# Optimization experiments

Hardware: AMD Instinct MI355X
Metric: run time of the kernel (lower is better)

## Reference

```python
import jax, jax.numpy as jnp
import numpy as np
import math

N_HEAD = 16
ROPE_BASE = 10000.0


def _rope_cos_sin(seq_len, head_dim, dtype):
    # standard RoPE tables: freqs_i = base^(-2i/d), i in [0, d/2)
    half = head_dim // 2
    inv_freq = ROPE_BASE ** (-(jnp.arange(half, dtype=jnp.float32) * 2.0 / head_dim))
    t = jnp.arange(seq_len, dtype=jnp.float32)
    ang = t[:, None] * inv_freq[None, :]  # [S, d/2]
    return jnp.cos(ang).astype(dtype), jnp.sin(ang).astype(dtype)


def _apply_rope(x, cos, sin):
    # x: [B, S, H, d]; rotate interleaved even/odd pairs
    x1 = x[..., 0::2]
    x2 = x[..., 1::2]
    c = cos[None, :, None, :]
    s = sin[None, :, None, :]
    out = jnp.stack([x1 * c - x2 * s, x1 * s + x2 * c], axis=-1)
    return out.reshape(x.shape)


def setup_inputs() -> dict:
    key = jax.random.key(0)
    kx, kq, kk, kv, ko = jax.random.split(key, 5)
    B, S, H = 2, 2048, 1024
    x = jax.random.normal(kx, (B, S, H), dtype=jnp.float32)
    scale = 0.02
    w_q = jax.random.normal(kq, (H, H), dtype=jnp.float32) * scale
    w_k = jax.random.normal(kk, (H, H), dtype=jnp.float32) * scale
    w_v = jax.random.normal(kv, (H, H), dtype=jnp.float32) * scale
    w_o = jax.random.normal(ko, (H, H), dtype=jnp.float32) * scale
    return {"x": x, "w_q": w_q, "w_k": w_k, "w_v": w_v, "w_o": w_o}


def reference(x, w_q, w_k, w_v, w_o):
    B, S, H = x.shape
    d = H // N_HEAD
    # torch nn.Linear(bias=False): y = x @ W^T, W is [out, in]
    q = (x @ w_q.T).reshape(B, S, N_HEAD, d)
    k = (x @ w_k.T).reshape(B, S, N_HEAD, d)
    v = (x @ w_v.T).reshape(B, S, N_HEAD, d)
    cos, sin = _rope_cos_sin(S, d, x.dtype)
    q = _apply_rope(q, cos, sin)
    k = _apply_rope(k, cos, sin)
    scores = jnp.einsum("bqhd,bkhd->bhqk", q, k) / math.sqrt(d)
    coefs = jax.nn.softmax(scores, axis=-1)
    # NOTE: causal mask is applied AFTER softmax via tril (no renormalization)
    causal = jnp.tril(jnp.ones((S, S), dtype=bool))
    coefs = jnp.where(causal[None, None], coefs, 0.0)
    out = jnp.einsum("bhqk,bkhd->bqhd", coefs, v).reshape(B, S, H)
    return out @ w_o.T
```

## Files before the change

kernel.cpp:

```cpp
#include <hip/hip_runtime.h>
#include <math.h>

#define SEQ   2048
#define HDIM  1024
#define NH    16
#define DH    64
#define MTOT  4096
#define BHTOT 32

typedef _Float16 half_t;
typedef __attribute__((ext_vector_type(2))) __fp16 fp16x2;
typedef __attribute__((ext_vector_type(4))) _Float16 half4;
typedef __attribute__((ext_vector_type(8))) _Float16 half8;
typedef __attribute__((ext_vector_type(4))) float float4v;

typedef __attribute__((address_space(1))) const unsigned int guint;
typedef __attribute__((address_space(3))) unsigned int luint;
__device__ __forceinline__ void glds16(const half_t* g, half_t* l) {
    __builtin_amdgcn_global_load_lds((guint*)g, (luint*)l, 16, 0, 0);
}

__global__ __launch_bounds__(256)
void prep(const float* __restrict__ x,  const float* __restrict__ wq,
          const float* __restrict__ wk, const float* __restrict__ wv,
          const float* __restrict__ wo,
          half_t* __restrict__ xh,  half_t* __restrict__ wqh,
          half_t* __restrict__ wkh, half_t* __restrict__ wvh,
          half_t* __restrict__ woh, float2* __restrict__ rope)
{
    const int bid = blockIdx.x;
    if (bid < 8192) {
        int i = bid * 256 + threadIdx.x;
        const float* s; half_t* d;
        if (i < 1048576) { s = x; d = xh; }
        else {
            int j = i - 1048576;
            int w = j >> 18; i = j & 262143;
            s = (w == 0) ? wq : (w == 1) ? wk : (w == 2) ? wv : wo;
            d = (w == 0) ? wqh : (w == 1) ? wkh : (w == 2) ? wvh : woh;
        }
        float4 v = ((const float4*)s)[i];
        union { half_t h[4]; uint2 u; } tmp;
        tmp.h[0] = (half_t)v.x; tmp.h[1] = (half_t)v.y;
        tmp.h[2] = (half_t)v.z; tmp.h[3] = (half_t)v.w;
        ((uint2*)d)[i] = tmp.u;
    } else {
        int tt = (bid - 8192) * 256 + threadIdx.x;
        int s = tt >> 5, j = tt & 31;
        float inv = powf(10000.0f, -(float)j / 32.0f);
        float ang = (float)s * inv;
        rope[tt] = make_float2(cosf(ang), sinf(ang));
    }
}

__global__ __launch_bounds__(256, 5)
void gemm_qkv(const half_t* __restrict__ A,
              const half_t* __restrict__ w0, const half_t* __restrict__ w1,
              const half_t* __restrict__ w2,
              half_t* __restrict__ Qb, half_t* __restrict__ Kb,
              half_t* __restrict__ Vtb,
              const float2* __restrict__ rope)
{
    const int mode = blockIdx.z;
    const half_t* Bw = (mode == 1) ? w1 : (mode == 2) ? w2 : w0;

    __shared__ __align__(16) half_t Tsh[2][128][64];
    half_t (*Ash)[64] = Tsh[0];
    half_t (*Bsh)[64] = Tsh[1];

    const int t    = threadIdx.x;
    const int lane = t & 63;
    const int wave = t >> 6;
    const int quad = lane >> 4;
    const int l16  = lane & 15;
    const int wr   = (wave >> 1) * 64;
    const int wc   = (wave & 1) * 64;
    const int bm   = blockIdx.x, bn = blockIdx.y;

    const int srow   = lane >> 3;
    const int schunk = (lane & 7) ^ (srow & 3);
    const half_t* Asrc = A  + (size_t)(bm * 128 + srow) * HDIM + schunk * 8;
    const half_t* Bsrc = Bw + (size_t)(bn * 128 + srow) * HDIM + schunk * 8;
    const int swz = (l16 & 3) << 4;

    float4v acc[4][4] = {};

    for (int kt = 0; kt < HDIM / 64; ++kt) {
        const half_t* Ak = Asrc + kt * 64;
        const half_t* Bk = Bsrc + kt * 64;
#pragma unroll
        for (int c = 0; c < 4; ++c) {
            const int r8 = wave * 32 + c * 8;
            glds16(Ak + (size_t)r8 * HDIM, &Ash[r8][0]);
            glds16(Bk + (size_t)r8 * HDIM, &Bsh[r8][0]);
        }
        __syncthreads();
#pragma unroll
        for (int kk = 0; kk < 2; ++kk) {
            const int cb = ((quad << 4) | (kk << 6)) ^ swz;
            half8 af[4], bf[4];
#pragma unroll
            for (int mb = 0; mb < 4; ++mb)
                af[mb] = *(const half8*)((const char*)&Ash[wr + mb * 16 + l16][0] + cb);
#pragma unroll
            for (int nb = 0; nb < 4; ++nb)
                bf[nb] = *(const half8*)((const char*)&Bsh[wc + nb * 16 + l16][0] + cb);
#pragma unroll
            for (int mb = 0; mb < 4; ++mb)
#pragma unroll
                for (int nb = 0; nb < 4; ++nb)
                    acc[mb][nb] = __builtin_amdgcn_mfma_f32_16x16x32_f16(af[mb], bf[nb], acc[mb][nb], 0, 0, 0);
        }
        __syncthreads();
    }

    if (mode == 2) {
#pragma unroll
        for (int mb = 0; mb < 4; ++mb)
#pragma unroll
            for (int nb = 0; nb < 4; ++nb) {
                int row0 = bm * 128 + wr + mb * 16 + quad * 4;
                int col  = bn * 128 + wc + nb * 16 + l16;
                int b = row0 >> 11, s0 = row0 & 2047;
                int h = col >> 6,  dd = col & 63;
                union { half_t h4[4]; uint2 u; } tmp;
#pragma unroll
                for (int r = 0; r < 4; ++r) tmp.h4[r] = (half_t)acc[mb][nb][r];
                *(uint2*)&Vtb[((size_t)((b * NH + h) * DH + dd)) * SEQ + s0] = tmp.u;
            }
        return;
    }
    {
        half_t* Ob = (mode == 0) ? Qb : Kb;
        const float scl = (mode == 0) ? 0.125f * 1.44269504088896f : 1.0f;
        const int h = (bn * 128 + wc) >> 6;
        float* E = (float*)&Tsh[0][0][0] + wave * 1088;
#pragma unroll
        for (int mb = 0; mb < 4; ++mb) {
#pragma unroll
            for (int nb = 0; nb < 4; ++nb)
#pragma unroll
                for (int r = 0; r < 4; ++r)
                    E[(quad * 4 + r) * 68 + nb * 16 + l16] = acc[mb][nb][r];
            __asm__ volatile("s_waitcnt lgkmcnt(0)" ::: "memory");
#pragma unroll
            for (int c = 0; c < 2; ++c) {
                const int uidx = c * 64 + lane;
                const int row = uidx >> 3, ch = uidx & 7;
                const int sg = bm * 128 + wr + mb * 16 + row;
                const int b = sg >> 11, s = sg & 2047;
                const float* Er = E + row * 68 + ch * 8;
                const float4 e0 = *(const float4*)Er;
                const float4 e1 = *(const float4*)(Er + 4);
                const float4* rp = (const float4*)(rope + (size_t)s * 32 + ch * 4);
                const float4 r01 = rp[0];
                const float4 r23 = rp[1];
                union { half_t hh[8]; uint4 u; } o;
                o.hh[0] = (half_t)((e0.x * r01.x - e0.y * r01.y) * scl);
                o.hh[1] = (half_t)((e0.x * r01.y + e0.y * r01.x) * scl);
                o.hh[2] = (half_t)((e0.z * r01.z - e0.w * r01.w) * scl);
                o.hh[3] = (half_t)((e0.z * r01.w + e0.w * r01.z) * scl);
                o.hh[4] = (half_t)((e1.x * r23.x - e1.y * r23.y) * scl);
                o.hh[5] = (half_t)((e1.x * r23.y + e1.y * r23.x) * scl);
                o.hh[6] = (half_t)((e1.z * r23.z - e1.w * r23.w) * scl);
                o.hh[7] = (half_t)((e1.z * r23.w + e1.w * r23.z) * scl);
                *(uint4*)&Ob[((size_t)((b * NH + h) * SEQ + s)) * DH + ch * 8] = o.u;
            }
        }
    }
}

__global__ __launch_bounds__(256)
void gemm_out(const half_t* __restrict__ A, const half_t* __restrict__ W,
              float* __restrict__ outF)
{
    __shared__ __align__(16) half_t Ash[2][64][64];
    __shared__ __align__(16) half_t Bsh[2][64][64];

    const int t    = threadIdx.x;
    const int lane = t & 63;
    const int wave = t >> 6;
    const int quad = lane >> 4;
    const int l16  = lane & 15;
    const int wr   = (wave >> 1) * 32;
    const int wc   = (wave & 1) * 32;
    const int bm   = blockIdx.x, bn = blockIdx.y;

    const int srow   = lane >> 3;
    const int schunk = (lane & 7) ^ (srow & 3);
    const half_t* Asrc = A + (size_t)(bm * 64 + srow) * HDIM + schunk * 8;
    const half_t* Bsrc = W + (size_t)(bn * 64 + srow) * HDIM + schunk * 8;
    const int swz = (l16 & 3) << 4;

    auto stage = [&](int kt, int buf) {
        const half_t* Ak = Asrc + kt * 64;
        const half_t* Bk = Bsrc + kt * 64;
#pragma unroll
        for (int c = 0; c < 2; ++c) {
            const int r8 = wave * 16 + c * 8;
            glds16(Ak + (size_t)r8 * HDIM, &Ash[buf][r8][0]);
            glds16(Bk + (size_t)r8 * HDIM, &Bsh[buf][r8][0]);
        }
    };

    float4v acc[2][2] = {};

    stage(0, 0);
    __asm__ volatile("s_waitcnt vmcnt(0)" ::: "memory");
    __builtin_amdgcn_s_barrier();
    __builtin_amdgcn_sched_barrier(0);

    for (int kt = 0; kt < HDIM / 64; ++kt) {
        const int cur = kt & 1, nxt = cur ^ 1;
        if (kt + 1 < HDIM / 64) stage(kt + 1, nxt);
#pragma unroll
        for (int kk = 0; kk < 2; ++kk) {
            const int cb = ((quad << 4) | (kk << 6)) ^ swz;
            half8 af[2], bf[2];
#pragma unroll
            for (int mb = 0; mb < 2; ++mb)
                af[mb] = *(const half8*)((const char*)&Ash[cur][wr + mb * 16 + l16][0] + cb);
#pragma unroll
            for (int nb = 0; nb < 2; ++nb)
                bf[nb] = *(const half8*)((const char*)&Bsh[cur][wc + nb * 16 + l16][0] + cb);
#pragma unroll
            for (int mb = 0; mb < 2; ++mb)
#pragma unroll
                for (int nb = 0; nb < 2; ++nb)
                    acc[mb][nb] = __builtin_amdgcn_mfma_f32_16x16x32_f16(af[mb], bf[nb], acc[mb][nb], 0, 0, 0);
        }
        __asm__ volatile("s_waitcnt vmcnt(0)" ::: "memory");
        __builtin_amdgcn_s_barrier();
        __builtin_amdgcn_sched_barrier(0);
    }

#pragma unroll
    for (int mb = 0; mb < 2; ++mb)
#pragma unroll
        for (int nb = 0; nb < 2; ++nb) {
            int row0 = bm * 64 + wr + mb * 16 + quad * 4;
            int col  = bn * 64 + wc + nb * 16 + l16;
#pragma unroll
            for (int r = 0; r < 4; ++r)
                outF[(size_t)(row0 + r) * HDIM + col] = acc[mb][nb][r];
        }
}

__global__ __launch_bounds__(512, 2)
void attn_fused(const half_t* __restrict__ Qb, const half_t* __restrict__ Kb,
                const half_t* __restrict__ Vtb, half_t* __restrict__ AOut)
{
    const int p  = blockIdx.y >> 2;
    const int bh = (blockIdx.y & 3) * 8 + blockIdx.x;
    const int NT = SEQ / 128;

    __shared__ __align__(16) half_t Ksh[2][128][64];
    __shared__ __align__(16) half_t Vsh[2][64][128];

    const int t = threadIdx.x;
    const int wave = t >> 6, lane = t & 63, quad = lane >> 4, l16 = lane & 15;
    const int q0g[2] = { p * 128 + wave * 16, (15 - p) * 128 + wave * 16 };
    const int vtop = 15 - p;

    half8 qf0[2], qf1[2];
#pragma unroll
    for (int g = 0; g < 2; ++g) {
        const half_t* Qp = Qb + ((size_t)bh * SEQ + q0g[g] + l16) * DH + quad * 8;
        qf0[g] = *(const half8*)Qp;
        qf1[g] = *(const half8*)(Qp + 32);
    }

    float4v o0[4] = {}, o1[4] = {};
    float4v ls0 = {}, ls1 = {};

    const int krow = lane >> 3, kpos = lane & 7;
    const int kchunk = kpos ^ krow;
    const half_t* Ksrc = Kb + ((size_t)bh * SEQ + wave * 16 + krow) * DH + kchunk * 8;
    const int ko1 = ((quad ^ (l16 & 7)) * 8);
    const int ko2 = ko1 ^ 32;

    const int sr  = t >> 3;
    const int sc0 = t & 7;
    const half_t* Vg = Vtb + ((size_t)bh * DH + sr) * SEQ + sc0 * 8;
    const int vso0 = ((sc0    ) ^ (sr & 15)) * 8;
    const int vso1 = ((sc0 + 8) ^ (sr & 15)) * 8;

    {
        uint4 va0 = *(const uint4*)(Vg);
        uint4 va1 = *(const uint4*)(Vg + 64);
        glds16(Ksrc,          &Ksh[0][wave * 16][0]);
        glds16(Ksrc + 8 * DH, &Ksh[0][wave * 16 + 8][0]);
        *(uint4*)&Vsh[0][sr][vso0] = va0;
        *(uint4*)&Vsh[0][sr][vso1] = va1;
    }
    __asm__ volatile("s_waitcnt vmcnt(0)" ::: "memory");
    __asm__ volatile("s_waitcnt lgkmcnt(0)" ::: "memory");
    __builtin_amdgcn_s_barrier();
    __builtin_amdgcn_sched_barrier(0);

    for (int T = 0; T < NT; ++T) {
        const int cur = T & 1, nxt = cur ^ 1;
        const bool kn = (T + 1 < NT);
        const bool vn = kn && (T + 1 <= vtop);

        uint4 va0, va1;
        if (vn) {
            va0 = *(const uint4*)(Vg + (T + 1) * 128);
            va1 = *(const uint4*)(Vg + (T + 1) * 128 + 64);
        }
        if (kn) {
            const half_t* Kn = Ksrc + (size_t)(T + 1) * 128 * DH;
            glds16(Kn,          &Ksh[nxt][wave * 16][0]);
            glds16(Kn + 8 * DH, &Ksh[nxt][wave * 16 + 8][0]);
        }

#pragma unroll
        for (int hh = 0; hh < 2; ++hh) {
            float4v s0[4], s1[4];
            __builtin_amdgcn_s_setprio(1);
#pragma unroll
            for (int nb = 0; nb < 4; ++nb) {
                const half_t* kp = &Ksh[cur][hh * 64 + nb * 16 + l16][0];
                half8 kf0 = *(const half8*)(kp + ko1);
                half8 kf1 = *(const half8*)(kp + ko2);
                float4v a = {};
                a = __builtin_amdgcn_mfma_f32_16x16x32_f16(kf0, qf0[0], a, 0, 0, 0);
                a = __builtin_amdgcn_mfma_f32_16x16x32_f16(kf1, qf1[0], a, 0, 0, 0);
                s0[nb] = a;
                float4v b = {};
                b = __builtin_amdgcn_mfma_f32_16x16x32_f16(kf0, qf0[1], b, 0, 0, 0);
                b = __builtin_amdgcn_mfma_f32_16x16x32_f16(kf1, qf1[1], b, 0, 0, 0);
                s1[nb] = b;
            }
            __builtin_amdgcn_s_setprio(0);

#pragma unroll
            for (int nb = 0; nb < 4; ++nb)
#pragma unroll
                for (int r = 0; r < 4; ++r) {
                    float e0 = __builtin_amdgcn_exp2f(s0[nb][r]);
                    float e1 = __builtin_amdgcn_exp2f(s1[nb][r]);
                    s0[nb][r] = e0; ls0[r] += e0;
                    s1[nb][r] = e1; ls1[r] += e1;
                }

            const int kbase = T * 128 + hh * 64;
            const bool act0 = (kbase <= q0g[0] + 15);
            const bool act1 = (kbase <= q0g[1] + 15);
            if (act1) {
                if (kbase + 63 > q0g[1]) {
                    int qg = q0g[1] + l16;
#pragma unroll
                    for (int nb = 0; nb < 4; ++nb)
#pragma unroll
                        for (int r = 0; r < 4; ++r)
                            if (kbase + nb * 16 + quad * 4 + r > qg) s1[nb][r] = 0.f;
                }
                if (act0 && kbase + 63 > q0g[0]) {
                    int qg = q0g[0] + l16;
#pragma unroll
                    for (int nb = 0; nb < 4; ++nb)
#pragma unroll
                        for (int r = 0; r < 4; ++r)
                            if (kbase + nb * 16 + quad * 4 + r > qg) s0[nb][r] = 0.f;
                }
                half4 pf1[4], pf0[4];
#pragma unroll
                for (int nb = 0; nb < 4; ++nb) {
                    union { fp16x2 v2[2]; half4 v4; } u;
                    u.v2[0] = __builtin_amdgcn_cvt_pkrtz(s1[nb][0], s1[nb][1]);
                    u.v2[1] = __builtin_amdgcn_cvt_pkrtz(s1[nb][2], s1[nb][3]);
                    pf1[nb] = u.v4;
                }
                if (act0) {
#pragma unroll
                    for (int nb = 0; nb < 4; ++nb) {
                        union { fp16x2 v2[2]; half4 v4; } u;
                        u.v2[0] = __builtin_amdgcn_cvt_pkrtz(s0[nb][0], s0[nb][1]);
                        u.v2[1] = __builtin_amdgcn_cvt_pkrtz(s0[nb][2], s0[nb][3]);
                        pf0[nb] = u.v4;
                    }
                }
                __builtin_amdgcn_s_setprio(1);
                if (act0) {
#pragma unroll
                    for (int md = 0; md < 4; ++md) {
                        const char* vrow = (const char*)&Vsh[cur][md * 16 + l16][0];
#pragma unroll
                        for (int nb = 0; nb < 4; ++nb) {
                            const int chunk = (hh * 8 + nb * 2 + (quad >> 1)) ^ l16;
                            half4 vf = *(const half4*)(vrow + chunk * 16 + (quad & 1) * 8);
                            o1[md] = __builtin_amdgcn_mfma_f32_16x16x16f16(vf, pf1[nb], o1[md], 0, 0, 0);
                            o0[md] = __builtin_amdgcn_mfma_f32_16x16x16f16(vf, pf0[nb], o0[md], 0, 0, 0);
                        }
                    }
                } else {
#pragma unroll
                    for (int md = 0; md < 4; ++md) {
                        const char* vrow = (const char*)&Vsh[cur][md * 16 + l16][0];
#pragma unroll
                        for (int nb = 0; nb < 4; ++nb) {
                            const int chunk = (hh * 8 + nb * 2 + (quad >> 1)) ^ l16;
                            half4 vf = *(const half4*)(vrow + chunk * 16 + (quad & 1) * 8);
                            o1[md] = __builtin_amdgcn_mfma_f32_16x16x16f16(vf, pf1[nb], o1[md], 0, 0, 0);
                        }
                    }
                }
                __builtin_amdgcn_s_setprio(0);
            }
        }

        if (vn) {
            *(uint4*)&Vsh[nxt][sr][vso0] = va0;
            *(uint4*)&Vsh[nxt][sr][vso1] = va1;
        }
        __asm__ volatile("s_waitcnt vmcnt(0)" ::: "memory");
        __asm__ volatile("s_waitcnt lgkmcnt(0)" ::: "memory");
        __builtin_amdgcn_s_barrier();
        __builtin_amdgcn_sched_barrier(0);
    }

    const int b = bh >> 4, h = bh & 15;
    const int orow = lane >> 2, occ = (lane & 3) * 16;
    half_t* scr = (half_t*)Ksh + wave * 1152;
    half_t (*Osh)[72] = (half_t(*)[72])scr;
#pragma unroll
    for (int g = 0; g < 2; ++g) {
        const float4v& lsg = g ? ls1 : ls0;
        float rs = (lsg[0] + lsg[1]) + (lsg[2] + lsg[3]);
        rs += __shfl_xor(rs, 16, 64);
        rs += __shfl_xor(rs, 32, 64);
        const float inv = 1.0f / rs;
#pragma unroll
        for (int md = 0; md < 4; ++md)
#pragma unroll
            for (int r = 0; r < 4; ++r)
                Osh[l16][md * 16 + quad * 4 + r] =
                    (half_t)(((g ? o1 : o0)[md][r]) * inv);
        __asm__ volatile("s_waitcnt lgkmcnt(0)" ::: "memory");
        uint4 v0 = *(const uint4*)&Osh[orow][occ];
        uint4 v1 = *(const uint4*)&Osh[orow][occ + 8];
        const int s = q0g[g] + orow;
        half_t* dst = AOut + ((size_t)(b * SEQ + s)) * HDIM + h * DH + occ;
        *(uint4*)dst       = v0;
        *(uint4*)(dst + 8) = v1;
    }
}

extern "C" void kernel_launch(void* const* d_in, const int* in_sizes, int n_in,
                              void* d_out, int out_size, void* d_ws, size_t ws_size,
                              hipStream_t stream)
{
    const float* x  = (const float*)d_in[0];
    const float* wq = (const float*)d_in[1];
    const float* wk = (const float*)d_in[2];
    const float* wv = (const float*)d_in[3];
    const float* wo = (const float*)d_in[4];
    float* out = (float*)d_out;

    char* ws = (char*)d_ws;
    size_t off = 0;
    auto alloc = [&](size_t bytes) -> void* {
        void* p = ws + off;
        off += (bytes + 255) & ~(size_t)255;
        return p;
    };
    half_t* xh   = (half_t*)alloc((size_t)MTOT * HDIM * 2);
    half_t* wqh  = (half_t*)alloc((size_t)HDIM * HDIM * 2);
    half_t* wkh  = (half_t*)alloc((size_t)HDIM * HDIM * 2);
    half_t* wvh  = (half_t*)alloc((size_t)HDIM * HDIM * 2);
    half_t* woh  = (half_t*)alloc((size_t)HDIM * HDIM * 2);
    half_t* Qb   = (half_t*)alloc((size_t)BHTOT * SEQ * DH * 2);
    half_t* Kb   = (half_t*)alloc((size_t)BHTOT * SEQ * DH * 2);
    half_t* Vtb  = (half_t*)alloc((size_t)BHTOT * SEQ * DH * 2);
    half_t* ah   = (half_t*)alloc((size_t)MTOT * HDIM * 2);
    float2* rope = (float2*)alloc((size_t)SEQ * 32 * sizeof(float2));

    prep<<<8448, 256, 0, stream>>>(x, wq, wk, wv, wo, xh, wqh, wkh, wvh, woh, rope);

    gemm_qkv<<<dim3(32, 8, 3), 256, 0, stream>>>(xh, wqh, wkh, wvh,
                                                 Qb, Kb, Vtb, rope);
    attn_fused<<<dim3(8, 32), 512, 0, stream>>>(Qb, Kb, Vtb, ah);
    gemm_out<<<dim3(64, 16), 256, 0, stream>>>(ah, woh, out);
}
```

Measured before the change: 186.2 us.

## Double-buffer QKV GEMM K-loop and split attention blocks into smaller 4-wave tiles

The QKV GEMM now stages 32-wide K slices into double-buffered LDS, prefetching the next slice while computing on the current one. This replaces the load-sync-compute-sync loop and cuts the barriers per iteration from two to one. The attention kernel moves from 512-thread blocks over 128-key tiles to 256-thread blocks over 64-key tiles. It launches twice as many blocks, with each query pair split into halves, and drops the XOR swizzle on V in favour of a padded row stride of 72. The aim is better latency hiding and occupancy, at the risk of more LDS bank conflicts and more per-tile sync overhead.

```diff
diff --git a/kernel.cpp b/kernel.cpp
--- a/kernel.cpp
+++ b/kernel.cpp
@@ -64,9 +64,7 @@
     const int mode = blockIdx.z;
     const half_t* Bw = (mode == 1) ? w1 : (mode == 2) ? w2 : w0;
 
-    __shared__ __align__(16) half_t Tsh[2][128][64];
-    half_t (*Ash)[64] = Tsh[0];
-    half_t (*Bsh)[64] = Tsh[1];
+    __shared__ __align__(16) half_t Tsh[2][2][128][32];
 
     const int t    = threadIdx.x;
     const int lane = t & 63;
@@ -77,41 +75,47 @@
     const int wc   = (wave & 1) * 64;
     const int bm   = blockIdx.x, bn = blockIdx.y;
 
-    const int srow   = lane >> 3;
-    const int schunk = (lane & 7) ^ (srow & 3);
+    const int srow   = lane >> 2;
+    const int schunk = (lane & 3) ^ (srow & 3);
     const half_t* Asrc = A  + (size_t)(bm * 128 + srow) * HDIM + schunk * 8;
     const half_t* Bsrc = Bw + (size_t)(bn * 128 + srow) * HDIM + schunk * 8;
     const int swz = (l16 & 3) << 4;
 
+    auto stage = [&](int kt, int buf) {
+        const half_t* Ak = Asrc + kt * 32;
+        const half_t* Bk = Bsrc + kt * 32;
+        glds16(Ak + (size_t)(wave * 32)      * HDIM, &Tsh[buf][0][wave * 32][0]);
+        glds16(Ak + (size_t)(wave * 32 + 16) * HDIM, &Tsh[buf][0][wave * 32 + 16][0]);
+        glds16(Bk + (size_t)(wave * 32)      * HDIM, &Tsh[buf][1][wave * 32][0]);
+        glds16(Bk + (size_t)(wave * 32 + 16) * HDIM, &Tsh[buf][1][wave * 32 + 16][0]);
+    };
+
     float4v acc[4][4] = {};
 
-    for (int kt = 0; kt < HDIM / 64; ++kt) {
-        const half_t* Ak = Asrc + kt * 64;
-        const half_t* Bk = Bsrc + kt * 64;
-#pragma unroll
-        for (int c = 0; c < 4; ++c) {
-            const int r8 = wave * 32 + c * 8;
-            glds16(Ak + (size_t)r8 * HDIM, &Ash[r8][0]);
-            glds16(Bk + (size_t)r8 * HDIM, &Bsh[r8][0]);
-        }
-        __syncthreads();
-#pragma unroll
-        for (int kk = 0; kk < 2; ++kk) {
-            const int cb = ((quad << 4) | (kk << 6)) ^ swz;
-            half8 af[4], bf[4];
-#pragma unroll
-            for (int mb = 0; mb < 4; ++mb)
-                af[mb] = *(const half8*)((const char*)&Ash[wr + mb * 16 + l16][0] + cb);
+    stage(0, 0);
+    __asm__ volatile("s_waitcnt vmcnt(0)" ::: "memory");
+    __builtin_amdgcn_s_barrier();
+    __builtin_amdgcn_sched_barrier(0);
+
+    for (int kt = 0; kt < HDIM / 32; ++kt) {
+        const int cur = kt & 1, nxt = cur ^ 1;
+        if (kt + 1 < HDIM / 32) stage(kt + 1, nxt);
+        const int cb = (quad << 4) ^ swz;
+        half8 af[4], bf[4];
+#pragma unroll
+        for (int mb = 0; mb < 4; ++mb)
+            af[mb] = *(const half8*)((const char*)&Tsh[cur][0][wr + mb * 16 + l16][0] + cb);
+#pragma unroll
+        for (int nb = 0; nb < 4; ++nb)
+            bf[nb] = *(const half8*)((const char*)&Tsh[cur][1][wc + nb * 16 + l16][0] + cb);
+#pragma unroll
+        for (int mb = 0; mb < 4; ++mb)
 #pragma unroll
             for (int nb = 0; nb < 4; ++nb)
-                bf[nb] = *(const half8*)((const char*)&Bsh[wc + nb * 16 + l16][0] + cb);
-#pragma unroll
-            for (int mb = 0; mb < 4; ++mb)
-#pragma unroll
-                for (int nb = 0; nb < 4; ++nb)
-                    acc[mb][nb] = __builtin_amdgcn_mfma_f32_16x16x32_f16(af[mb], bf[nb], acc[mb][nb], 0, 0, 0);
-        }
-        __syncthreads();
+                acc[mb][nb] = __builtin_amdgcn_mfma_f32_16x16x32_f16(af[mb], bf[nb], acc[mb][nb], 0, 0, 0);
+        __asm__ volatile("s_waitcnt vmcnt(0)" ::: "memory");
+        __builtin_amdgcn_s_barrier();
+        __builtin_amdgcn_sched_barrier(0);
     }
 
     if (mode == 2) {
@@ -134,7 +138,7 @@
         half_t* Ob = (mode == 0) ? Qb : Kb;
         const float scl = (mode == 0) ? 0.125f * 1.44269504088896f : 1.0f;
         const int h = (bn * 128 + wc) >> 6;
-        float* E = (float*)&Tsh[0][0][0] + wave * 1088;
+        float* E = (float*)&Tsh[0][0][0][0] + wave * 1088;
 #pragma unroll
         for (int mb = 0; mb < 4; ++mb) {
 #pragma unroll
@@ -246,21 +250,24 @@
         }
 }
 
-__global__ __launch_bounds__(512, 2)
+__global__ __launch_bounds__(256, 2)
 void attn_fused(const half_t* __restrict__ Qb, const half_t* __restrict__ Kb,
                 const half_t* __restrict__ Vtb, half_t* __restrict__ AOut)
 {
-    const int p  = blockIdx.y >> 2;
-    const int bh = (blockIdx.y & 3) * 8 + blockIdx.x;
-    const int NT = SEQ / 128;
-
-    __shared__ __align__(16) half_t Ksh[2][128][64];
-    __shared__ __align__(16) half_t Vsh[2][64][128];
+    const int bx = blockIdx.x;
+    const int p  = bx >> 1;
+    const int hf = bx & 1;
+    const int bh = blockIdx.y;
+    const int NT = SEQ / 64;
+
+    __shared__ __align__(16) half_t Ksh[2][64][64];
+    __shared__ __align__(16) half_t Vsh[2][64][72];
 
     const int t = threadIdx.x;
     const int wave = t >> 6, lane = t & 63, quad = lane >> 4, l16 = lane & 15;
-    const int q0g[2] = { p * 128 + wave * 16, (15 - p) * 128 + wave * 16 };
-    const int vtop = 15 - p;
+    const int q0g[2] = { p * 128 + hf * 64 + wave * 16,
+                         (15 - p) * 128 + hf * 64 + wave * 16 };
+    const int ktop = 2 * (15 - p) + hf;
 
     half8 qf0[2], qf1[2];
 #pragma unroll
@@ -279,19 +286,17 @@
     const int ko1 = ((quad ^ (l16 & 7)) * 8);
     const int ko2 = ko1 ^ 32;
 
-    const int sr  = t >> 3;
-    const int sc0 = t & 7;
-    const half_t* Vg = Vtb + ((size_t)bh * DH + sr) * SEQ + sc0 * 8;
-    const int vso0 = ((sc0    ) ^ (sr & 15)) * 8;
-    const int vso1 = ((sc0 + 8) ^ (sr & 15)) * 8;
+    const int sr  = t >> 2;
+    const int scc = (t & 3) * 16;
+    const half_t* Vg = Vtb + ((size_t)bh * DH + sr) * SEQ + scc;
 
     {
-        uint4 va0 = *(const uint4*)(Vg);
-        uint4 va1 = *(const uint4*)(Vg + 64);
+        uint4 va = *(const uint4*)(Vg);
+        uint4 vb = *(const uint4*)(Vg + 8);
         glds16(Ksrc,          &Ksh[0][wave * 16][0]);
         glds16(Ksrc + 8 * DH, &Ksh[0][wave * 16 + 8][0]);
-        *(uint4*)&Vsh[0][sr][vso0] = va0;
-        *(uint4*)&Vsh[0][sr][vso1] = va1;
+        *(uint4*)&Vsh[0][sr][scc]     = va;
+        *(uint4*)&Vsh[0][sr][scc + 8] = vb;
     }
     __asm__ volatile("s_waitcnt vmcnt(0)" ::: "memory");
     __asm__ volatile("s_waitcnt lgkmcnt(0)" ::: "memory");
@@ -301,118 +306,110 @@
     for (int T = 0; T < NT; ++T) {
         const int cur = T & 1, nxt = cur ^ 1;
         const bool kn = (T + 1 < NT);
-        const bool vn = kn && (T + 1 <= vtop);
-
-        uint4 va0, va1;
+        const bool vn = kn && (T + 1 <= ktop);
+
+        uint4 va, vb;
         if (vn) {
-            va0 = *(const uint4*)(Vg + (T + 1) * 128);
-            va1 = *(const uint4*)(Vg + (T + 1) * 128 + 64);
+            const half_t* Vgk = Vg + (T + 1) * 64;
+            va = *(const uint4*)(Vgk);
+            vb = *(const uint4*)(Vgk + 8);
         }
         if (kn) {
-            const half_t* Kn = Ksrc + (size_t)(T + 1) * 128 * DH;
+            const half_t* Kn = Ksrc + (size_t)(T + 1) * 64 * DH;
             glds16(Kn,          &Ksh[nxt][wave * 16][0]);
             glds16(Kn + 8 * DH, &Ksh[nxt][wave * 16 + 8][0]);
         }
 
-#pragma unroll
-        for (int hh = 0; hh < 2; ++hh) {
-            float4v s0[4], s1[4];
-            __builtin_amdgcn_s_setprio(1);
+        float4v s0[4], s1[4];
+        __builtin_amdgcn_s_setprio(1);
+#pragma unroll
+        for (int nb = 0; nb < 4; ++nb) {
+            const half_t* kp = &Ksh[cur][nb * 16 + l16][0];
+            half8 kf0 = *(const half8*)(kp + ko1);
+            half8 kf1 = *(const half8*)(kp + ko2);
+            float4v a = {};
+            a = __builtin_amdgcn_mfma_f32_16x16x32_f16(kf0, qf0[0], a, 0, 0, 0);
+            a = __builtin_amdgcn_mfma_f32_16x16x32_f16(kf1, qf1[0], a, 0, 0, 0);
+            s0[nb] = a;
+            float4v b = {};
+            b = __builtin_amdgcn_mfma_f32_16x16x32_f16(kf0, qf0[1], b, 0, 0, 0);
+            b = __builtin_amdgcn_mfma_f32_16x16x32_f16(kf1, qf1[1], b, 0, 0, 0);
+            s1[nb] = b;
+        }
+        __builtin_amdgcn_s_setprio(0);
+
+#pragma unroll
+        for (int nb = 0; nb < 4; ++nb)
+#pragma unroll
+            for (int r = 0; r < 4; ++r) {
+                float e0 = __builtin_amdgcn_exp2f(s0[nb][r]);
+                float e1 = __builtin_amdgcn_exp2f(s1[nb][r]);
+                s0[nb][r] = e0; ls0[r] += e0;
+                s1[nb][r] = e1; ls1[r] += e1;
+            }
+
+        const int kbase = T * 64;
+        const bool act0 = (kbase <= q0g[0] + 15);
+        const bool act1 = (kbase <= q0g[1] + 15);
+        if (act1) {
+            if (kbase + 63 > q0g[1]) {
+                int qg = q0g[1] + l16;
+#pragma unroll
+                for (int nb = 0; nb < 4; ++nb)
+#pragma unroll
+                    for (int r = 0; r < 4; ++r)
+                        if (kbase + nb * 16 + quad * 4 + r > qg) s1[nb][r] = 0.f;
+            }
+            if (act0 && kbase + 63 > q0g[0]) {
+                int qg = q0g[0] + l16;
+#pragma unroll
+                for (int nb = 0; nb < 4; ++nb)
+#pragma unroll
+                    for (int r = 0; r < 4; ++r)
+                        if (kbase + nb * 16 + quad * 4 + r > qg) s0[nb][r] = 0.f;
+            }
+            half4 pf1[4], pf0[4];
 #pragma unroll
             for (int nb = 0; nb < 4; ++nb) {
-                const half_t* kp = &Ksh[cur][hh * 64 + nb * 16 + l16][0];
-                half8 kf0 = *(const half8*)(kp + ko1);
-                half8 kf1 = *(const half8*)(kp + ko2);
-                float4v a = {};
-                a = __builtin_amdgcn_mfma_f32_16x16x32_f16(kf0, qf0[0], a, 0, 0, 0);
-                a = __builtin_amdgcn_mfma_f32_16x16x32_f16(kf1, qf1[0], a, 0, 0, 0);
-                s0[nb] = a;
-                float4v b = {};
-                b = __builtin_amdgcn_mfma_f32_16x16x32_f16(kf0, qf0[1], b, 0, 0, 0);
-                b = __builtin_amdgcn_mfma_f32_16x16x32_f16(kf1, qf1[1], b, 0, 0, 0);
-                s1[nb] = b;
-            }
-            __builtin_amdgcn_s_setprio(0);
-
-#pragma unroll
-            for (int nb = 0; nb < 4; ++nb)
-#pragma unroll
-                for (int r = 0; r < 4; ++r) {
-                    float e0 = __builtin_amdgcn_exp2f(s0[nb][r]);
-                    float e1 = __builtin_amdgcn_exp2f(s1[nb][r]);
-                    s0[nb][r] = e0; ls0[r] += e0;
-                    s1[nb][r] = e1; ls1[r] += e1;
-                }
-
-            const int kbase = T * 128 + hh * 64;
-            const bool act0 = (kbase <= q0g[0] + 15);
-            const bool act1 = (kbase <= q0g[1] + 15);
-            if (act1) {
-                if (kbase + 63 > q0g[1]) {
-                    int qg = q0g[1] + l16;
-#pragma unroll
-                    for (int nb = 0; nb < 4; ++nb)
-#pragma unroll
-                        for (int r = 0; r < 4; ++r)
-                            if (kbase + nb * 16 + quad * 4 + r > qg) s1[nb][r] = 0.f;
-                }
-                if (act0 && kbase + 63 > q0g[0]) {
-                    int qg = q0g[0] + l16;
-#pragma unroll
-                    for (int nb = 0; nb < 4; ++nb)
-#pragma unroll
-                        for (int r = 0; r < 4; ++r)
-                            if (kbase + nb * 16 + quad * 4 + r > qg) s0[nb][r] = 0.f;
-                }
-                half4 pf1[4], pf0[4];
+                union { fp16x2 v2[2]; half4 v4; } u;
+                u.v2[0] = __builtin_amdgcn_cvt_pkrtz(s1[nb][0], s1[nb][1]);
+                u.v2[1] = __builtin_amdgcn_cvt_pkrtz(s1[nb][2], s1[nb][3]);
+                pf1[nb] = u.v4;
+            }
+            if (act0) {
 #pragma unroll
                 for (int nb = 0; nb < 4; ++nb) {
                     union { fp16x2 v2[2]; half4 v4; } u;
-                    u.v2[0] = __builtin_amdgcn_cvt_pkrtz(s1[nb][0], s1[nb][1]);
-                    u.v2[1] = __builtin_amdgcn_cvt_pkrtz(s1[nb][2], s1[nb][3]);
-                    pf1[nb] = u.v4;
+                    u.v2[0] = __builtin_amdgcn_cvt_pkrtz(s0[nb][0], s0[nb][1]);
+                    u.v2[1] = __builtin_amdgcn_cvt_pkrtz(s0[nb][2], s0[nb][3]);
+                    pf0[nb] = u.v4;
                 }
-                if (act0) {
+            }
+            __builtin_amdgcn_s_setprio(1);
+            if (act0) {
+#pragma unroll
+                for (int md = 0; md < 4; ++md)
 #pragma unroll
                     for (int nb = 0; nb < 4; ++nb) {
-                        union { fp16x2 v2[2]; half4 v4; } u;
-                        u.v2[0] = __builtin_amdgcn_cvt_pkrtz(s0[nb][0], s0[nb][1]);
-                        u.v2[1] = __builtin_amdgcn_cvt_pkrtz(s0[nb][2], s0[nb][3]);
-                        pf0[nb] = u.v4;
+                        half4 vf = *(const half4*)&Vsh[cur][md * 16 + l16][nb * 16 + quad * 4];
+                        o1[md] = __builtin_amdgcn_mfma_f32_16x16x16f16(vf, pf1[nb], o1[md], 0, 0, 0);
+                        o0[md] = __builtin_amdgcn_mfma_f32_16x16x16f16(vf, pf0[nb], o0[md], 0, 0, 0);
                     }
-                }
-                __builtin_amdgcn_s_setprio(1);
-                if (act0) {
-#pragma unroll
-                    for (int md = 0; md < 4; ++md) {
-                        const char* vrow = (const char*)&Vsh[cur][md * 16 + l16][0];
-#pragma unroll
-                        for (int nb = 0; nb < 4; ++nb) {
-                            const int chunk = (hh * 8 + nb * 2 + (quad >> 1)) ^ l16;
-                            half4 vf = *(const half4*)(vrow + chunk * 16 + (quad & 1) * 8);
-                            o1[md] = __builtin_amdgcn_mfma_f32_16x16x16f16(vf, pf1[nb], o1[md], 0, 0, 0);
-                            o0[md] = __builtin_amdgcn_mfma_f32_16x16x16f16(vf, pf0[nb], o0[md], 0, 0, 0);
-                        }
+            } else {
+#pragma unroll
+                for (int md = 0; md < 4; ++md)
+#pragma unroll
+                    for (int nb = 0; nb < 4; ++nb) {
+                        half4 vf = *(const half4*)&Vsh[cur][md * 16 + l16][nb * 16 + quad * 4];
+                        o1[md] = __builtin_amdgcn_mfma_f32_16x16x16f16(vf, pf1[nb], o1[md], 0, 0, 0);
                     }
-                } else {
-#pragma unroll
-                    for (int md = 0; md < 4; ++md) {
-                        const char* vrow = (const char*)&Vsh[cur][md * 16 + l16][0];
-#pragma unroll
-                        for (int nb = 0; nb < 4; ++nb) {
-                            const int chunk = (hh * 8 + nb * 2 + (quad >> 1)) ^ l16;
-                            half4 vf = *(const half4*)(vrow + chunk * 16 + (quad & 1) * 8);
-                            o1[md] = __builtin_amdgcn_mfma_f32_16x16x16f16(vf, pf1[nb], o1[md], 0, 0, 0);
-                        }
-                    }
-                }
-                __builtin_amdgcn_s_setprio(0);
-            }
+            }
+            __builtin_amdgcn_s_setprio(0);
         }
 
         if (vn) {
-            *(uint4*)&Vsh[nxt][sr][vso0] = va0;
-            *(uint4*)&Vsh[nxt][sr][vso1] = va1;
+            *(uint4*)&Vsh[nxt][sr][scc]     = va;
+            *(uint4*)&Vsh[nxt][sr][scc + 8] = vb;
         }
         __asm__ volatile("s_waitcnt vmcnt(0)" ::: "memory");
         __asm__ volatile("s_waitcnt lgkmcnt(0)" ::: "memory");
@@ -480,6 +477,6 @@
 
     gemm_qkv<<<dim3(32, 8, 3), 256, 0, stream>>>(xh, wqh, wkh, wvh,
                                                  Qb, Kb, Vtb, rope);
-    attn_fused<<<dim3(8, 32), 512, 0, stream>>>(Qb, Kb, Vtb, ah);
+    attn_fused<<<dim3(16, 32), 256, 0, stream>>>(Qb, Kb, Vtb, ah);
     gemm_out<<<dim3(64, 16), 256, 0, stream>>>(ah, woh, out);
 }
```

New measurement: 188.8 us. Within noise of the previous version (+1.4%).
